# Performance work log

Measured on AMD Instinct MI355X. Metric: run time of the kernel, lower is better.

## Reference

```python
import jax, jax.numpy as jnp
import numpy as np

NEG_BIG = -9e15

def mish(x):
    return x * jnp.tanh(jax.nn.softplus(x))

def setup_inputs() -> dict:
    key = jax.random.key(0)
    k1, k2, k3, k4 = jax.random.split(key, 4)
    N, Fin, Fout = 8192, 512, 256
    x = jax.random.normal(k1, (N, Fin), dtype=jnp.float32)
    adj = jax.random.randint(k2, (N, N), 0, 2, dtype=jnp.int32)
    # xavier-uniform-like params
    wlim = np.sqrt(6.0 / (Fin + Fout)).astype(np.float32)
    weight = jax.random.uniform(k3, (Fin, Fout), dtype=jnp.float32, minval=-wlim, maxval=wlim)
    alim = np.sqrt(6.0 / (2 * Fout + 1)).astype(np.float32)
    a = jax.random.uniform(k4, (2 * Fout, 1), dtype=jnp.float32, minval=-alim, maxval=alim)
    return {"x": x, "adj": adj, "weight": weight, "a": a}

def reference(x, adj, weight, a):
    Fout = weight.shape[1]
    h = x @ weight                      # [N, Fout]
    # e[i,j] = mish(h_i . a1 + h_j . a2) -- avoids O(N^2 * 2F) a_input
    s_src = h @ a[:Fout, 0]             # [N]
    s_dst = h @ a[Fout:, 0]             # [N]
    e = mish(s_src[:, None] + s_dst[None, :])  # [N, N]
    logits = jnp.where(adj > 0, e, NEG_BIG)
    attention = jax.nn.softmax(logits, axis=1)  # dropout skipped (eval mode)
    h_prime = attention @ h             # [N, Fout]
    return mish(h_prime)
```

## Files before the change

### kernel.cpp

```cpp
#include <hip/hip_runtime.h>
#include <hip/hip_fp16.h>

#define NROWS 8192
#define FIN   512
#define FOUT  256
#define BM    64

using f16   = _Float16;
using f16x8 = __attribute__((ext_vector_type(8))) f16;
using f16x4 = __attribute__((ext_vector_type(4))) f16;
using f32x4 = __attribute__((ext_vector_type(4))) float;
using i32x4 = __attribute__((ext_vector_type(4))) int;

#define MFMA16(a, b, c) __builtin_amdgcn_mfma_f32_16x16x32_f16((a), (b), (c), 0, 0, 0)

__device__ __forceinline__ float mish_f(float x) {
  float t = __expf(x);
  float u = t * (t + 2.0f);
  return x * (u / (u + 2.0f));
}

__device__ __forceinline__ float dot4(float4 p, float4 q) {
  return p.x * q.x + p.y * q.y + p.z * q.z + p.w * q.w;
}

__global__ __launch_bounds__(256) void k0_prep(
    const float* __restrict__ wgt, const float* __restrict__ a,
    f16* __restrict__ wB_hi, f16* __restrict__ wB_lo,
    float* __restrict__ wa1, float* __restrict__ wa2) {
  int k = blockIdx.x, f = threadIdx.x;
  float v = wgt[(size_t)k * FOUT + f];
  int kt = k >> 5, g2 = (k >> 3) & 3, e = k & 7;
  size_t base = (((size_t)(kt * 16 + (f >> 4)) * 64) + g2 * 16 + (f & 15)) * 8 + e;
  f16 h = (f16)v;
  wB_hi[base] = h;
  wB_lo[base] = (f16)(v - (float)h);

  float p1 = v * a[f], p2 = v * a[FOUT + f];
  for (int off = 32; off > 0; off >>= 1) {
    p1 += __shfl_down(p1, off);
    p2 += __shfl_down(p2, off);
  }
  __shared__ float red[8];
  int w = threadIdx.x >> 6, lane = threadIdx.x & 63;
  if (lane == 0) { red[w] = p1; red[4 + w] = p2; }
  __syncthreads();
  if (threadIdx.x == 0) {
    wa1[k] = red[0] + red[1] + red[2] + red[3];
    wa2[k] = red[4] + red[5] + red[6] + red[7];
  }
}

__global__ __launch_bounds__(256) void k2_scores(
    const float* __restrict__ x, const float* __restrict__ wa1,
    const float* __restrict__ wa2, float* __restrict__ s_src,
    float* __restrict__ s_dst, unsigned int* __restrict__ maxd_enc) {
  int wv = threadIdx.x >> 6, lane = threadIdx.x & 63;
  int row = blockIdx.x * 4 + wv;
  const float4* xr = (const float4*)(x + (size_t)row * FIN);
  float4 x0 = xr[lane * 2], x1 = xr[lane * 2 + 1];
  const float4* w1 = (const float4*)wa1;
  const float4* w2 = (const float4*)wa2;
  float p1 = dot4(x0, w1[lane * 2]) + dot4(x1, w1[lane * 2 + 1]);
  float p2 = dot4(x0, w2[lane * 2]) + dot4(x1, w2[lane * 2 + 1]);
  for (int off = 32; off > 0; off >>= 1) {
    p1 += __shfl_down(p1, off);
    p2 += __shfl_down(p2, off);
  }
  if (lane == 0) {
    s_src[row] = p1;
    s_dst[row] = p2;
    unsigned b = __float_as_uint(p2);
    unsigned enc = (b & 0x80000000u) ? ~b : (b | 0x80000000u);
    atomicMax(maxd_enc, enc);
  }
}

__global__ __launch_bounds__(256) void k1_gemm_h(
    const float* __restrict__ x, const f16* __restrict__ wB_hi,
    const f16* __restrict__ wB_lo, f16* __restrict__ hB_hi,
    f16* __restrict__ hB_lo) {
  __shared__ float xs[64][36];
  int mt = blockIdx.x >> 1, ns = blockIdx.x & 1;
  int m0 = mt * 64;
  int tid = threadIdx.x;
  int w = tid >> 6, lane = tid & 63;
  int g = lane >> 4, lr = lane & 15;

  f32x4 acc[4][2] = {};

  for (int kk = 0; kk < FIN; kk += 32) {
    {
      int r = tid >> 3;
      int c = (tid & 7) * 4;
      *(float4*)(&xs[r][c])      = *(const float4*)(x + (size_t)(m0 + r) * FIN + kk + c);
      *(float4*)(&xs[r + 32][c]) = *(const float4*)(x + (size_t)(m0 + r + 32) * FIN + kk + c);
    }
    __syncthreads();
    int kt = kk >> 5;
    f16x8 bh[2], bl[2];
#pragma unroll
    for (int ct = 0; ct < 2; ++ct) {
      int ft = ns * 8 + w * 2 + ct;
      size_t slot = ((size_t)(kt * 16 + ft) * 64 + lane) * 8;
      bh[ct] = *(const f16x8*)(wB_hi + slot);
      bl[ct] = *(const f16x8*)(wB_lo + slot);
    }
#pragma unroll
    for (int rt = 0; rt < 4; ++rt) {
      const float* ap = &xs[rt * 16 + lr][g * 8];
      f16x8 ah, al;
#pragma unroll
      for (int e = 0; e < 8; ++e) {
        float v = ap[e];
        f16 h = (f16)v;
        ah[e] = h;
        al[e] = (f16)(v - (float)h);
      }
#pragma unroll
      for (int ct = 0; ct < 2; ++ct) {
        acc[rt][ct] = MFMA16(ah, bh[ct], acc[rt][ct]);
        acc[rt][ct] = MFMA16(ah, bl[ct], acc[rt][ct]);
        acc[rt][ct] = MFMA16(al, bh[ct], acc[rt][ct]);
      }
    }
    __syncthreads();
  }

#pragma unroll
  for (int rt = 0; rt < 4; ++rt) {
    int jg0 = m0 + rt * 16 + g * 4;
    int jt = jg0 >> 5, g2 = (jg0 >> 3) & 3, e0 = jg0 & 7;
#pragma unroll
    for (int ct = 0; ct < 2; ++ct) {
      int f = ns * 128 + w * 32 + ct * 16 + lr;
      size_t base = (((size_t)(jt * 16 + (f >> 4)) * 64) + g2 * 16 + (f & 15)) * 8 + e0;
      f16x4 hv, lv;
#pragma unroll
      for (int rg = 0; rg < 4; ++rg) {
        float v = acc[rt][ct][rg];
        f16 h = (f16)v;
        hv[rg] = h;
        lv[rg] = (f16)(v - (float)h);
      }
      *(f16x4*)(hB_hi + base) = hv;
      *(f16x4*)(hB_lo + base) = lv;
    }
  }
}

__global__ __launch_bounds__(256, 4) void k3_attn(
    const int* __restrict__ adj, const f16* __restrict__ hB_hi,
    const f16* __restrict__ hB_lo, const float* __restrict__ s_src,
    const float* __restrict__ s_dst, const unsigned int* __restrict__ maxd_enc,
    float* __restrict__ npart, float* __restrict__ zpart, int shift) {
  extern __shared__ char smem[];
  const int CH = NROWS >> shift;
  const int NG = CH >> 6;
  float* sd = (float*)smem;
  f16*   pb = (f16*)(smem + CH * 4);
  float* zl = (float*)(smem + CH * 4 + 16384);

  int tid = threadIdx.x;
  int lane = tid & 63;
  int w = tid >> 6;
  int q = w;
  int r = lane;
  int jc = blockIdx.x & ((1 << shift) - 1);
  int ib = blockIdx.x >> shift;
  int i0 = ib * BM;
  int j0 = jc * CH;

  for (int u = tid; u < (CH >> 2); u += 256)
    *(float4*)(&sd[u * 4]) = *(const float4*)(s_dst + j0 + u * 4);

  unsigned enc = *maxd_enc;
  float maxd = (enc & 0x80000000u) ? __uint_as_float(enc & 0x7fffffffu)
                                   : __uint_as_float(~enc);
  int row = i0 + r;
  float s_i = s_src[row];
  float m_i = fmaxf(0.f, s_i + maxd);
  const int* aptr = adj + (size_t)row * NROWS + j0 + q * 16;

  __syncthreads();

  f32x4 acc[4][4] = {};
  float zacc = 0.f;

  int sg_w = q >> 1;
  int g16a = (q & 1) * 2;
  int lane_r = r & 15;
  int rt_w = r >> 4;

  i32x4 cur[4], nxt[4];
#pragma unroll
  for (int u = 0; u < 4; ++u) cur[u] = *(const i32x4*)(aptr + u * 4);

  for (int g = 0; g < NG; ++g) {
    int buf = g & 1;
    f16x8 v0, v1;
#pragma unroll
    for (int u = 0; u < 4; ++u) {
      float4 sdv = *(const float4*)(&sd[g * 64 + q * 16 + u * 4]);
      float sa[4] = {sdv.x, sdv.y, sdv.z, sdv.w};
#pragma unroll
      for (int c = 0; c < 4; ++c) {
        float s = s_i + sa[c];
        float t = __expf(s);
        float uu = t * (t + 2.0f);
        float sc = s * (uu / (uu + 2.0f));
        float p = __expf(sc - m_i);
        f16 pf = (cur[u][c] != 0) ? (f16)p : (f16)0.0f;
        zacc += (float)pf;
        if (u < 2) v0[u * 4 + c] = pf;
        else       v1[(u - 2) * 4 + c] = pf;
      }
    }
    {
      size_t sbase = ((size_t)(buf * 2 + sg_w) * 4 + rt_w) * 64;
      *(f16x8*)(pb + (sbase + (size_t)g16a * 16 + lane_r) * 8)       = v0;
      *(f16x8*)(pb + (sbase + (size_t)(g16a + 1) * 16 + lane_r) * 8) = v1;
    }
    __syncthreads();

    if (g + 1 < NG) {
#pragma unroll
      for (int u = 0; u < 4; ++u)
        nxt[u] = *(const i32x4*)(aptr + (size_t)(g + 1) * 64 + u * 4);
    }

    int jtb = (j0 + g * 64) >> 5;
#pragma unroll
    for (int sg = 0; sg < 2; ++sg) {
      int jt = jtb + sg;
      f16x8 afr[4];
#pragma unroll
      for (int rt = 0; rt < 4; ++rt)
        afr[rt] = *(const f16x8*)(pb +
            (((size_t)(buf * 2 + sg) * 4 + rt) * 64 + lane) * 8);
#pragma unroll
      for (int ct = 0; ct < 4; ++ct) {
        int ft = w * 4 + ct;
        size_t slot = ((size_t)(jt * 16 + ft) * 64 + lane) * 8;
        f16x8 bh = *(const f16x8*)(hB_hi + slot);
        f16x8 bl = *(const f16x8*)(hB_lo + slot);
#pragma unroll
        for (int rt = 0; rt < 4; ++rt) {
          acc[rt][ct] = MFMA16(afr[rt], bh, acc[rt][ct]);
          acc[rt][ct] = MFMA16(afr[rt], bl, acc[rt][ct]);
        }
      }
    }
#pragma unroll
    for (int u = 0; u < 4; ++u) cur[u] = nxt[u];
  }

  zl[tid] = zacc;
  __syncthreads();
  if (tid < 64) {
    float z = zl[tid] + zl[64 + tid] + zl[128 + tid] + zl[192 + tid];
    zpart[(size_t)jc * NROWS + i0 + tid] = z;
  }

  float* np = npart + ((size_t)jc * NROWS + i0) * FOUT;
#pragma unroll
  for (int rt = 0; rt < 4; ++rt)
#pragma unroll
    for (int ct = 0; ct < 4; ++ct)
#pragma unroll
      for (int rg = 0; rg < 4; ++rg) {
        int rr = rt * 16 + (lane >> 4) * 4 + rg;
        int cc = w * 64 + ct * 16 + (lane & 15);
        np[(size_t)rr * FOUT + cc] = acc[rt][ct][rg];
      }
}

__global__ __launch_bounds__(256) void k5_reduce(
    const float* __restrict__ npart, const float* __restrict__ zpart,
    float* __restrict__ out, int njc) {
  int gid = blockIdx.x * 256 + threadIdx.x;
  int row = gid >> 6;
  int c4 = (gid & 63) * 4;
  float z = 0.f;
  for (int j = 0; j < njc; ++j) z += zpart[(size_t)j * NROWS + row];
  float4 s = {0.f, 0.f, 0.f, 0.f};
  for (int j = 0; j < njc; ++j) {
    float4 v = *(const float4*)(npart + ((size_t)j * NROWS + row) * FOUT + c4);
    s.x += v.x; s.y += v.y; s.z += v.z; s.w += v.w;
  }
  float rz = 1.0f / z;
  s.x = mish_f(s.x * rz);
  s.y = mish_f(s.y * rz);
  s.z = mish_f(s.z * rz);
  s.w = mish_f(s.w * rz);
  *(float4*)(out + (size_t)row * FOUT + c4) = s;
}

extern "C" void kernel_launch(void* const* d_in, const int* in_sizes, int n_in,
                              void* d_out, int out_size, void* d_ws, size_t ws_size,
                              hipStream_t stream) {
  const float* x   = (const float*)d_in[0];
  const int*   adj = (const int*)d_in[1];
  const float* wgt = (const float*)d_in[2];
  const float* a   = (const float*)d_in[3];
  float* out = (float*)d_out;

  char* ws = (char*)d_ws;
  f16* hB_hi = (f16*)ws;
  f16* hB_lo = (f16*)(ws + (4u << 20));
  f16* wB_hi = (f16*)(ws + (8u << 20));
  f16* wB_lo = (f16*)(ws + (8u << 20) + (256u << 10));
  float* wa1   = (float*)(ws + (8u << 20) + (512u << 10));
  float* wa2   = wa1 + FIN;
  float* s_src = wa2 + FIN;
  float* s_dst = s_src + NROWS;
  unsigned int* maxd = (unsigned int*)(s_dst + NROWS);
  float* zpart = (float*)wB_hi;

  size_t base = 9u << 20;
  int shift;
  if      (ws_size >= base + (64u << 20)) shift = 3;
  else if (ws_size >= base + (32u << 20)) shift = 2;
  else if (ws_size >= base + (16u << 20)) shift = 1;
  else shift = 0;
  int njc = 1 << shift;
  float* npart;
  if (ws_size >= base + ((size_t)njc << 23)) npart = (float*)(ws + base);
  else npart = out;

  (void)hipMemsetAsync(maxd, 0, sizeof(unsigned int), stream);

  k0_prep<<<FIN, 256, 0, stream>>>(wgt, a, wB_hi, wB_lo, wa1, wa2);
  k2_scores<<<NROWS / 4, 256, 0, stream>>>(x, wa1, wa2, s_src, s_dst, maxd);
  k1_gemm_h<<<(NROWS / 64) * 2, 256, 0, stream>>>(x, wB_hi, wB_lo, hB_hi, hB_lo);

  int CH = NROWS >> shift;
  size_t shmem = (size_t)CH * 4 + 16384 + 1024 + 16;
  k3_attn<<<(NROWS / BM) << shift, 256, shmem, stream>>>(
      adj, hB_hi, hB_lo, s_src, s_dst, maxd, npart, zpart, shift);
  k5_reduce<<<NROWS * FOUT / 4 / 256, 256, 0, stream>>>(npart, zpart, out, njc);
}
```

Measured before the change: 596.4 us.

## Drop hi/lo split of h and replace mish-exp with LUT interpolation

Stores h as a single fp16 array instead of hi/lo fp16 pairs, which halves the B-operand loads and the MFMA count in the attention kernel. The per-element mish plus exp is replaced by a shared-memory lookup table over [-16,16) with linear interpolation, scaled by a per-row exp(-m_i). The table clamps scores outside that range and adds interpolation error. Dropping the low half of h also lowers precision, so accuracy may fall below tolerance.

After: 573.5 us. -3.8%, faster.

```diff
diff --git a/kernel.cpp b/kernel.cpp
--- a/kernel.cpp
+++ b/kernel.cpp
@@ -78,8 +78,7 @@
 
 __global__ __launch_bounds__(256) void k1_gemm_h(
     const float* __restrict__ x, const f16* __restrict__ wB_hi,
-    const f16* __restrict__ wB_lo, f16* __restrict__ hB_hi,
-    f16* __restrict__ hB_lo) {
+    const f16* __restrict__ wB_lo, f16* __restrict__ hB) {
   __shared__ float xs[64][36];
   int mt = blockIdx.x >> 1, ns = blockIdx.x & 1;
   int m0 = mt * 64;
@@ -135,31 +134,26 @@
     for (int ct = 0; ct < 2; ++ct) {
       int f = ns * 128 + w * 32 + ct * 16 + lr;
       size_t base = (((size_t)(jt * 16 + (f >> 4)) * 64) + g2 * 16 + (f & 15)) * 8 + e0;
-      f16x4 hv, lv;
-#pragma unroll
-      for (int rg = 0; rg < 4; ++rg) {
-        float v = acc[rt][ct][rg];
-        f16 h = (f16)v;
-        hv[rg] = h;
-        lv[rg] = (f16)(v - (float)h);
-      }
-      *(f16x4*)(hB_hi + base) = hv;
-      *(f16x4*)(hB_lo + base) = lv;
+      f16x4 hv;
+#pragma unroll
+      for (int rg = 0; rg < 4; ++rg) hv[rg] = (f16)acc[rt][ct][rg];
+      *(f16x4*)(hB + base) = hv;
     }
   }
 }
 
 __global__ __launch_bounds__(256, 4) void k3_attn(
-    const int* __restrict__ adj, const f16* __restrict__ hB_hi,
-    const f16* __restrict__ hB_lo, const float* __restrict__ s_src,
-    const float* __restrict__ s_dst, const unsigned int* __restrict__ maxd_enc,
+    const int* __restrict__ adj, const f16* __restrict__ hB,
+    const float* __restrict__ s_src, const float* __restrict__ s_dst,
+    const unsigned int* __restrict__ maxd_enc,
     float* __restrict__ npart, float* __restrict__ zpart, int shift) {
   extern __shared__ char smem[];
   const int CH = NROWS >> shift;
   const int NG = CH >> 6;
-  float* sd = (float*)smem;
-  f16*   pb = (f16*)(smem + CH * 4);
-  float* zl = (float*)(smem + CH * 4 + 16384);
+  float* lut = (float*)smem;
+  float* sd  = (float*)(smem + 16384);
+  f16*   pb  = (f16*)(smem + 16384 + CH * 4);
+  float* zl  = (float*)(smem + 16384 + CH * 4 + 16384);
 
   int tid = threadIdx.x;
   int lane = tid & 63;
@@ -171,6 +165,13 @@
   int i0 = ib * BM;
   int j0 = jc * CH;
 
+  for (int i = tid; i < 2048; i += 256) {
+    float s0 = (i - 1024) * 0.015625f;
+    float g0 = __expf(mish_f(s0));
+    float g1 = __expf(mish_f(s0 + 0.015625f));
+    lut[2 * i]     = g0;
+    lut[2 * i + 1] = g1 - g0;
+  }
   for (int u = tid; u < (CH >> 2); u += 256)
     *(float4*)(&sd[u * 4]) = *(const float4*)(s_dst + j0 + u * 4);
 
@@ -180,6 +181,7 @@
   int row = i0 + r;
   float s_i = s_src[row];
   float m_i = fmaxf(0.f, s_i + maxd);
+  float c_i = __expf(-m_i);
   const int* aptr = adj + (size_t)row * NROWS + j0 + q * 16;
 
   __syncthreads();
@@ -206,12 +208,15 @@
 #pragma unroll
       for (int c = 0; c < 4; ++c) {
         float s = s_i + sa[c];
-        float t = __expf(s);
-        float uu = t * (t + 2.0f);
-        float sc = s * (uu / (uu + 2.0f));
-        float p = __expf(sc - m_i);
-        f16 pf = (cur[u][c] != 0) ? (f16)p : (f16)0.0f;
-        zacc += (float)pf;
+        float fidx = __builtin_fmaf(s, 64.0f, 1024.0f);
+        fidx = fminf(fmaxf(fidx, 0.0f), 2046.99f);
+        int idx = (int)fidx;
+        float frac = fidx - (float)idx;
+        float2 ev = *(const float2*)(&lut[idx * 2]);
+        float p = __builtin_fmaf(frac, ev.y, ev.x) * c_i;
+        float pm = (cur[u][c] != 0) ? p : 0.0f;
+        zacc += pm;
+        f16 pf = (f16)pm;
         if (u < 2) v0[u * 4 + c] = pf;
         else       v1[(u - 2) * 4 + c] = pf;
       }
@@ -242,13 +247,10 @@
       for (int ct = 0; ct < 4; ++ct) {
         int ft = w * 4 + ct;
         size_t slot = ((size_t)(jt * 16 + ft) * 64 + lane) * 8;
-        f16x8 bh = *(const f16x8*)(hB_hi + slot);
-        f16x8 bl = *(const f16x8*)(hB_lo + slot);
-#pragma unroll
-        for (int rt = 0; rt < 4; ++rt) {
+        f16x8 bh = *(const f16x8*)(hB + slot);
+#pragma unroll
+        for (int rt = 0; rt < 4; ++rt)
           acc[rt][ct] = MFMA16(afr[rt], bh, acc[rt][ct]);
-          acc[rt][ct] = MFMA16(afr[rt], bl, acc[rt][ct]);
-        }
       }
     }
 #pragma unroll
@@ -306,11 +308,10 @@
   float* out = (float*)d_out;
 
   char* ws = (char*)d_ws;
-  f16* hB_hi = (f16*)ws;
-  f16* hB_lo = (f16*)(ws + (4u << 20));
-  f16* wB_hi = (f16*)(ws + (8u << 20));
-  f16* wB_lo = (f16*)(ws + (8u << 20) + (256u << 10));
-  float* wa1   = (float*)(ws + (8u << 20) + (512u << 10));
+  f16* hB    = (f16*)ws;
+  f16* wB_hi = (f16*)(ws + (4u << 20));
+  f16* wB_lo = (f16*)(ws + (4u << 20) + (256u << 10));
+  float* wa1   = (float*)(ws + (4u << 20) + (512u << 10));
   float* wa2   = wa1 + FIN;
   float* s_src = wa2 + FIN;
   float* s_dst = s_src + NROWS;
@@ -332,11 +333,11 @@
 
   k0_prep<<<FIN, 256, 0, stream>>>(wgt, a, wB_hi, wB_lo, wa1, wa2);
   k2_scores<<<NROWS / 4, 256, 0, stream>>>(x, wa1, wa2, s_src, s_dst, maxd);
-  k1_gemm_h<<<(NROWS / 64) * 2, 256, 0, stream>>>(x, wB_hi, wB_lo, hB_hi, hB_lo);
+  k1_gemm_h<<<(NROWS / 64) * 2, 256, 0, stream>>>(x, wB_hi, wB_lo, hB);
 
   int CH = NROWS >> shift;
-  size_t shmem = (size_t)CH * 4 + 16384 + 1024 + 16;
+  size_t shmem = 16384 + (size_t)CH * 4 + 16384 + 1024 + 16;
   k3_attn<<<(NROWS / BM) << shift, 256, shmem, stream>>>(
-      adj, hB_hi, hB_lo, s_src, s_dst, maxd, npart, zpart, shift);
+      adj, hB, s_src, s_dst, maxd, npart, zpart, shift);
   k5_reduce<<<NROWS * FOUT / 4 / 256, 256, 0, stream>>>(npart, zpart, out, njc);
 }
```
